# Kernel tuning notes

Hardware: AMD Instinct MI355X
Metric: run time of the kernel (lower is better)

## Reference

```python
import jax, jax.numpy as jnp
import numpy as np

DECAY = 0.99
EPSILON = 1e-05
COMMITMENT_COST = 0.25
N_TOKENS = 8192   # B * h * w = 8 * 32 * 32
EMBED_DIM = 4096
VOCAB = 8192


def setup_inputs() -> dict:
    key = jax.random.key(0)
    k1, k2, k3 = jax.random.split(key, 3)
    return {
        "inputs": jax.random.normal(k1, (N_TOKENS, EMBED_DIM), dtype=jnp.float32),
        "embedding": jax.random.normal(k2, (VOCAB, EMBED_DIM), dtype=jnp.float32),
        "ema_w": jax.random.normal(k3, (VOCAB, EMBED_DIM), dtype=jnp.float32),
        "ema_cluster_size": jnp.zeros((VOCAB,), dtype=jnp.float32),
    }


def reference(inputs, embedding, ema_w, ema_cluster_size):
    n_tokens = inputs.shape[0]
    vocab = embedding.shape[0]
    distances = (jnp.sum(inputs * inputs, axis=1, keepdims=True)
                 + jnp.sum(embedding * embedding, axis=1)
                 - 2.0 * jnp.matmul(inputs, embedding.T))
    encoding_indices = jnp.argmin(distances, axis=1)            # [N]
    # one-hot @ embedding == gather of codebook rows
    quantized = embedding[encoding_indices]                      # [N, D]
    # sum of one-hot encodings over tokens == per-code counts
    counts = jax.ops.segment_sum(jnp.ones((n_tokens,), inputs.dtype),
                                 encoding_indices, num_segments=vocab)  # [V]
    # EMA cluster-size update with Laplace smoothing
    new_cluster_size = ema_cluster_size * DECAY + (1.0 - DECAY) * counts
    n = jnp.sum(new_cluster_size)
    new_cluster_size = (new_cluster_size + EPSILON) / (n + vocab * EPSILON) * n
    # dw = encodings.T @ flat_input == scatter-add of inputs per code
    dw = jax.ops.segment_sum(inputs, encoding_indices, num_segments=vocab)  # [V, D]
    new_ema_w = ema_w * DECAY + (1.0 - DECAY) * dw
    new_embedding = new_ema_w / new_cluster_size[:, None]
    # commitment loss (codebook side detached)
    e_latent_loss = jnp.mean((jax.lax.stop_gradient(quantized) - inputs) ** 2)
    loss = COMMITMENT_COST * e_latent_loss
    # straight-through estimator
    quantized_st = inputs + jax.lax.stop_gradient(quantized - inputs)
    avg_probs = counts / n_tokens
    perplexity = jnp.exp(-jnp.sum(avg_probs * jnp.log(avg_probs + 1e-10)))
    return (loss, quantized_st, perplexity, encoding_indices[:, None],
            new_cluster_size, new_ema_w, new_embedding)
```

## Files before the change

### kernel.cpp

```cpp
#include <hip/hip_runtime.h>
#include <hip/hip_fp16.h>
#include <stdint.h>

typedef _Float16 f16;
typedef float f32x4 __attribute__((ext_vector_type(4)));
typedef int i32x4v __attribute__((ext_vector_type(4)));
typedef int i32x8v __attribute__((ext_vector_type(8)));
typedef unsigned long long u64;

#define N_TOK 8192
#define VOCAB 8192
#define DIM   4096
#define DELTA 64.0f

__device__ __forceinline__ void gload16(const void* g, void* l) {
    __builtin_amdgcn_global_load_lds(
        (const __attribute__((address_space(1))) unsigned int*)(uintptr_t)g,
        (__attribute__((address_space(3))) unsigned int*)(uintptr_t)l,
        16, 0, 0);
}

__device__ __forceinline__ float keyinv(unsigned k) {
    unsigned b = (k & 0x80000000u) ? (k ^ 0x80000000u) : ~k;
    return __uint_as_float(b);
}

__device__ __forceinline__ void ins2(u64& k1, u64& k2, u64 v) {
    if (v < k1) { k2 = k1; k1 = v; }
    else if (v < k2) { k2 = v; }
}

__global__ __launch_bounds__(256) void k_pack(const float* __restrict__ inputs,
                                              const float* __restrict__ embedding,
                                              char* __restrict__ apk, char* __restrict__ bpk,
                                              float* __restrict__ enorms,
                                              int* __restrict__ counts) {
    int b = blockIdx.x, t = threadIdx.x;
    bool isB = b >= N_TOK;
    int row = isB ? b - N_TOK : b;
    const float* src = (isB ? embedding : inputs) + (size_t)row * DIM;
    char* dst = (isB ? bpk : apk) + (size_t)row * DIM;
    double nrm = 0.0;
#pragma unroll
    for (int k = 0; k < 4; k++) {
        int d0 = t * 4 + 1024 * k;
        float4 v = *(const float4*)(src + d0);
        nrm += (double)v.x * v.x + (double)v.y * v.y
             + (double)v.z * v.z + (double)v.w * v.w;
        int packed = 0;
        packed = __builtin_amdgcn_cvt_pk_fp8_f32(v.x, v.y, packed, false);
        packed = __builtin_amdgcn_cvt_pk_fp8_f32(v.z, v.w, packed, true);
        int c = d0 & 127;
        int u = c >> 4;
        int p = ((u & 1) << 2) | (u >> 1);
        *(int*)(dst + (d0 & ~127) + (p << 4) + (c & 15)) = packed;
    }
    if (isB) {
        __shared__ double red[256];
        red[t] = nrm;
        __syncthreads();
        for (int off = 128; off > 0; off >>= 1) {
            if (t < off) red[t] += red[t + off];
            __syncthreads();
        }
        if (t == 0) {
            enorms[row] = (float)red[0];
            counts[row] = 0;
        }
    }
}

__global__ __launch_bounds__(256) void k_gemm(const char* __restrict__ apk,
                                              const char* __restrict__ bpk,
                                              const float* __restrict__ enorms,
                                              u64* __restrict__ cand) {
    __shared__ alignas(16) char lds[65536];
    int b = blockIdx.x;
    int x = b & 7, l = b >> 3;
    int bm = x * 8 + ((l >> 3) & 7);
    int bn = (l >> 6) * 8 + (l & 7);
    int tid = threadIdx.x;
    int lane = tid & 63, wid = tid >> 6;
    int wm = wid >> 1, wn = wid & 1;

    const char* srcs[8];
    unsigned lof[8];
#pragma unroll
    for (int e = 0; e < 8; e++) {
        int tile = e >> 2, q = e & 3;
        int s = q * 256 + tid;
        int r = s >> 3;
        int c16 = (s & 7) ^ (r & 7);
        int row = (tile ? bn : bm) * 128 + r;
        srcs[e] = (tile ? bpk : apk) + (size_t)row * DIM + c16 * 16;
        lof[e] = tile * 16384 + q * 4096 + wid * 1024;
    }

    f32x4 acc[4][4];
#pragma unroll
    for (int m = 0; m < 4; m++)
#pragma unroll
        for (int n = 0; n < 4; n++) acc[m][n] = (f32x4){0.f, 0.f, 0.f, 0.f};

    const int g = lane >> 4;
    const int ra = wm * 64 + (lane & 15);
    const int rb = wn * 64 + (lane & 15);

#define STAGE(buf) { _Pragma("unroll") for (int e = 0; e < 8; e++) { \
        gload16(srcs[e], &lds[(buf) * 32768u + lof[e]]); srcs[e] += 128; } }

    STAGE(0);

    for (int kt = 0; kt < 32; ++kt) {
        const unsigned cur = (kt & 1) ? 32768u : 0u;
        if (kt < 31) {
            STAGE((kt & 1) ^ 1);
            asm volatile("s_waitcnt vmcnt(8)" ::: "memory");
        } else {
            asm volatile("s_waitcnt vmcnt(0)" ::: "memory");
        }
        __builtin_amdgcn_sched_barrier(0);
        __builtin_amdgcn_s_barrier();
        __builtin_amdgcn_s_setprio(1);
        {
            i32x8v a8[4], b8[4];
#pragma unroll
            for (int m = 0; m < 4; m++) {
                int r = ra + m * 16;
                i32x4v lo = *(const i32x4v*)&lds[cur + r * 128 + ((g ^ (r & 7)) << 4)];
                i32x4v hi = *(const i32x4v*)&lds[cur + r * 128 + (((4 + g) ^ (r & 7)) << 4)];
                a8[m] = __builtin_shufflevector(lo, hi, 0, 1, 2, 3, 4, 5, 6, 7);
            }
#pragma unroll
            for (int n = 0; n < 4; n++) {
                int r = rb + n * 16;
                i32x4v lo = *(const i32x4v*)&lds[cur + 16384 + r * 128 + ((g ^ (r & 7)) << 4)];
                i32x4v hi = *(const i32x4v*)&lds[cur + 16384 + r * 128 + (((4 + g) ^ (r & 7)) << 4)];
                b8[n] = __builtin_shufflevector(lo, hi, 0, 1, 2, 3, 4, 5, 6, 7);
            }
#pragma unroll
            for (int m = 0; m < 4; m++)
#pragma unroll
                for (int n = 0; n < 4; n++)
                    acc[m][n] = __builtin_amdgcn_mfma_scale_f32_16x16x128_f8f6f4(
                        a8[m], b8[n], acc[m][n], 0, 0,
                        0, 0x7F7F7F7F, 0, 0x7F7F7F7F);
        }
        __builtin_amdgcn_s_setprio(0);
        __builtin_amdgcn_s_barrier();
    }
#undef STAGE

    float en[4];
    int colb = bn * 128 + wn * 64 + (lane & 15);
#pragma unroll
    for (int n = 0; n < 4; n++) en[n] = enorms[colb + n * 16];
#pragma unroll
    for (int m = 0; m < 4; m++) {
#pragma unroll
        for (int reg = 0; reg < 4; reg++) {
            u64 k1 = ~0ull, k2 = ~0ull;
#pragma unroll
            for (int n = 0; n < 4; n++) {
                float d = en[n] - 2.0f * acc[m][n][reg];
                unsigned bb = __float_as_uint(d);
                unsigned key = (bb & 0x80000000u) ? ~bb : (bb | 0x80000000u);
                ins2(k1, k2, ((u64)key << 32) | (unsigned)(colb + n * 16));
            }
#pragma unroll
            for (int msk = 1; msk < 16; msk <<= 1) {
                u64 o1 = __shfl_xor(k1, msk, 64);
                u64 o2 = __shfl_xor(k2, msk, 64);
                ins2(k1, k2, o1);
                ins2(k1, k2, o2);
            }
            if ((lane & 15) == 0) {
                int rowg = bm * 128 + wm * 64 + m * 16 + ((lane >> 4) << 2) + reg;
                size_t slot = ((size_t)rowg * 64 + bn) * 2 + wn;
                ulonglong2 v; v.x = k1; v.y = k2;
                *(ulonglong2*)&cand[slot * 2] = v;
            }
        }
    }
}

__global__ __launch_bounds__(256) void k_cand(const u64* __restrict__ cand,
                                              const float* __restrict__ enorms,
                                              const float* __restrict__ inputs,
                                              const float* __restrict__ embedding,
                                              float* __restrict__ o_idx,
                                              float* __restrict__ o_quant,
                                              float* __restrict__ partials,
                                              int* __restrict__ counts) {
    int tok = blockIdx.x, t = threadIdx.x;
    int lane = t & 63, w = t >> 6;
    __shared__ u64 redu[4];
    __shared__ float redf[4];
    __shared__ float pdot[64][4];
    __shared__ int clist[64];
    __shared__ int s_cnt;
    if (t == 0) s_cnt = 0;
    u64 e = cand[(size_t)tok * 256 + t];
    u64 v = e;
#pragma unroll
    for (int msk = 1; msk < 64; msk <<= 1) {
        u64 o = __shfl_xor(v, msk, 64);
        if (o < v) v = o;
    }
    if (lane == 0) redu[w] = v;
    __syncthreads();
    u64 m01 = redu[0] < redu[1] ? redu[0] : redu[1];
    u64 m23 = redu[2] < redu[3] ? redu[2] : redu[3];
    u64 mall = m01 < m23 ? m01 : m23;
    float dmin = keyinv((unsigned)(mall >> 32));
    float myd = keyinv((unsigned)(e >> 32));
    if (myd <= dmin + DELTA) {
        int p = atomicAdd(&s_cnt, 1);
        if (p < 64) clist[p] = (int)(unsigned)(e & 0xffffffffu);
    }
    __syncthreads();
    int nc = min(s_cnt, 64);

    const float* xrow = inputs + (size_t)tok * DIM;
    float4 xr4[4];
#pragma unroll
    for (int k = 0; k < 4; k++) xr4[k] = *(const float4*)(xrow + t * 4 + 1024 * k);

    for (int i = 0; i < nc; i++) {
        int c = clist[i];
        const float* erow = embedding + (size_t)c * DIM;
        float p = 0.f;
#pragma unroll
        for (int k = 0; k < 4; k++) {
            float4 e4 = *(const float4*)(erow + t * 4 + 1024 * k);
            p += xr4[k].x * e4.x + xr4[k].y * e4.y + xr4[k].z * e4.z + xr4[k].w * e4.w;
        }
#pragma unroll
        for (int msk = 1; msk < 64; msk <<= 1) p += __shfl_xor(p, msk, 64);
        if (lane == 0) pdot[i][w] = p;
    }
    __syncthreads();

    float best = 3.4e38f;
    int bcol = 0x7fffffff;
    for (int i = 0; i < nc; i++) {
        int c = clist[i];
        float dot = (pdot[i][0] + pdot[i][1]) + (pdot[i][2] + pdot[i][3]);
        float dist = enorms[c] - 2.0f * dot;
        if (dist < best || (dist == best && c < bcol)) { best = dist; bcol = c; }
    }
    const float* eb = embedding + (size_t)bcol * DIM;
    float* qrow = o_quant + (size_t)tok * DIM;
    float ls = 0.f;
#pragma unroll
    for (int k = 0; k < 4; k++) {
        int d = t * 4 + 1024 * k;
        float4 q4 = *(const float4*)(eb + d);
        qrow[d + 0] = q4.x; qrow[d + 1] = q4.y; qrow[d + 2] = q4.z; qrow[d + 3] = q4.w;
        float dx = q4.x - xr4[k].x, dy = q4.y - xr4[k].y;
        float dz = q4.z - xr4[k].z, dw = q4.w - xr4[k].w;
        ls += dx * dx + dy * dy + dz * dz + dw * dw;
    }
#pragma unroll
    for (int msk = 1; msk < 64; msk <<= 1) ls += __shfl_xor(ls, msk, 64);
    if (lane == 0) redf[w] = ls;
    __syncthreads();
    if (t == 0) {
        partials[tok] = (redf[0] + redf[1]) + (redf[2] + redf[3]);
        o_idx[tok] = (float)bcol;
        atomicAdd(&counts[bcol], 1);
    }
}

__global__ __launch_bounds__(1024) void k_cs(const int* __restrict__ counts,
                                             const float* __restrict__ ema_cs,
                                             float* __restrict__ o_ncs,
                                             float* __restrict__ o_perp) {
    __shared__ float red[1024];
    int t = threadIdx.x;
    float pre[8];
    float psum = 0.f, esum = 0.f;
#pragma unroll
    for (int k = 0; k < 8; k++) {
        int j = t * 8 + k;
        float c = (float)counts[j];
        float p = ema_cs[j] * 0.99f + 0.01f * c;
        pre[k] = p;
        psum += p;
        float ap = c * (1.0f / 8192.0f);
        esum += ap * logf(ap + 1e-10f);
    }
    red[t] = psum;
    __syncthreads();
    for (int off = 512; off > 0; off >>= 1) {
        if (t < off) red[t] += red[t + off];
        __syncthreads();
    }
    float n = red[0];
    __syncthreads();
    red[t] = esum;
    __syncthreads();
    for (int off = 512; off > 0; off >>= 1) {
        if (t < off) red[t] += red[t + off];
        __syncthreads();
    }
    if (t == 0) o_perp[0] = expf(-red[0]);
    float scale = n / (n + (float)VOCAB * 1e-5f);
#pragma unroll
    for (int k = 0; k < 8; k++) {
        int j = t * 8 + k;
        o_ncs[j] = (pre[k] + 1e-5f) * scale;
    }
}

__global__ __launch_bounds__(1024) void k_loss(const float* __restrict__ partials,
                                               float* __restrict__ o_loss) {
    __shared__ float red[1024];
    int t = threadIdx.x;
    float s = 0.f;
#pragma unroll
    for (int k = 0; k < 8; k++) s += partials[t * 8 + k];
    red[t] = s;
    __syncthreads();
    for (int off = 512; off > 0; off >>= 1) {
        if (t < off) red[t] += red[t + off];
        __syncthreads();
    }
    if (t == 0) o_loss[0] = 0.25f * red[0] / ((float)N_TOK * (float)DIM);
}

__global__ __launch_bounds__(256) void k_ema(const float* __restrict__ o_idx,
                                             const float* __restrict__ inputs,
                                             const float* __restrict__ ema_w,
                                             const float* __restrict__ o_ncs,
                                             float* __restrict__ o_neww,
                                             float* __restrict__ o_newemb) {
    int j = blockIdx.x, t = threadIdx.x;
    __shared__ int scan[256];
    __shared__ int list[256];
    __shared__ int s_total;
    int c = 0;
    for (int k = 0; k < 32; k++) {
        int tok = t * 32 + k;
        if ((int)o_idx[tok] == j) c++;
    }
    scan[t] = c;
    __syncthreads();
    for (int off = 1; off < 256; off <<= 1) {
        int add = (t >= off) ? scan[t - off] : 0;
        __syncthreads();
        scan[t] += add;
        __syncthreads();
    }
    int excl = scan[t] - c;
    if (t == 255) s_total = scan[255];
    __syncthreads();
    int pos = excl;
    for (int k = 0; k < 32; k++) {
        int tok = t * 32 + k;
        if ((int)o_idx[tok] == j && pos < 256) list[pos++] = tok;
    }
    __syncthreads();
    int total = s_total;
    float nc = o_ncs[j];
    size_t rowoff = (size_t)j * DIM;
#pragma unroll
    for (int k = 0; k < 4; k++) {
        int d = t * 4 + 1024 * k;
        float sx = 0.f, sy = 0.f, sz = 0.f, sw = 0.f;
        for (int q = 0; q < total; q++) {
            float4 v = *(const float4*)(inputs + (size_t)list[q] * DIM + d);
            sx += v.x; sy += v.y; sz += v.z; sw += v.w;
        }
        float4 w4 = *(const float4*)(ema_w + rowoff + d);
        float w0 = w4.x * 0.99f + 0.01f * sx;
        float w1 = w4.y * 0.99f + 0.01f * sy;
        float w2 = w4.z * 0.99f + 0.01f * sz;
        float w3 = w4.w * 0.99f + 0.01f * sw;
        o_neww[rowoff + d + 0] = w0; o_newemb[rowoff + d + 0] = w0 / nc;
        o_neww[rowoff + d + 1] = w1; o_newemb[rowoff + d + 1] = w1 / nc;
        o_neww[rowoff + d + 2] = w2; o_newemb[rowoff + d + 2] = w2 / nc;
        o_neww[rowoff + d + 3] = w3; o_newemb[rowoff + d + 3] = w3 / nc;
    }
}

extern "C" void kernel_launch(void* const* d_in, const int* in_sizes, int n_in,
                              void* d_out, int out_size, void* d_ws, size_t ws_size,
                              hipStream_t stream) {
    const float* inputs    = (const float*)d_in[0];
    const float* embedding = (const float*)d_in[1];
    const float* ema_w     = (const float*)d_in[2];
    const float* ema_cs    = (const float*)d_in[3];

    float* out = (float*)d_out;
    char* base = (char*)d_out;

    char* apk       = base;
    char* bpk       = base + 33554432;
    u64* cand       = (u64*)(base + 167772160);
    float* enorms   = (float*)(base + 184549376);
    int* counts     = (int*)(base + 184582144);
    float* partials = (float*)(base + 184614912);

    float* o_loss   = out;
    float* o_quant  = out + 1;
    float* o_perp   = out + 33554433;
    float* o_idx    = out + 33554434;
    float* o_ncs    = out + 33562626;
    float* o_neww   = out + 33570818;
    float* o_newemb = out + 67125250;

    k_pack<<<dim3(N_TOK + VOCAB), dim3(256), 0, stream>>>(inputs, embedding, apk, bpk,
                                                          enorms, counts);
    k_gemm<<<dim3(4096), dim3(256), 0, stream>>>(apk, bpk, enorms, cand);
    k_cand<<<dim3(N_TOK), dim3(256), 0, stream>>>(cand, enorms, inputs, embedding,
                                                  o_idx, o_quant, partials, counts);
    k_cs<<<dim3(1), dim3(1024), 0, stream>>>(counts, ema_cs, o_ncs, o_perp);
    k_loss<<<dim3(1), dim3(1024), 0, stream>>>(partials, o_loss);
    k_ema<<<dim3(VOCAB), dim3(256), 0, stream>>>(o_idx, inputs, ema_w, o_ncs, o_neww, o_newemb);
}
```

Before: 1.332 ms.

## Replace double-buffered FP8 GEMM K-loop with single-buffer 256-wide K tiles

The FP8 distance GEMM drops its two-stage LDS double buffer (128-byte K slices, explicit vmcnt waits, setprio) in favour of a single buffer holding 256-byte K slices. Each iteration loads the A and B tiles, synchronises, runs two MFMA half-steps, and synchronises again. This halves the loop count and barrier pairs and simplifies address arithmetic through a shared A/B pointer delta. In exchange, global loads no longer overlap with MFMA compute, so each iteration waits for its full load before computing.

```diff
diff --git a/kernel.cpp b/kernel.cpp
--- a/kernel.cpp
+++ b/kernel.cpp
@@ -87,14 +87,14 @@
     unsigned lof[8];
 #pragma unroll
     for (int e = 0; e < 8; e++) {
-        int tile = e >> 2, q = e & 3;
-        int s = q * 256 + tid;
-        int r = s >> 3;
-        int c16 = (s & 7) ^ (r & 7);
-        int row = (tile ? bn : bm) * 128 + r;
-        srcs[e] = (tile ? bpk : apk) + (size_t)row * DIM + c16 * 16;
-        lof[e] = tile * 16384 + q * 4096 + wid * 1024;
-    }
+        int s = e * 256 + tid;
+        int r = s >> 4;
+        int u = s & 15, h = u >> 3, j = u & 7;
+        int jp = j ^ (r & 7);
+        srcs[e] = apk + (size_t)(bm * 128 + r) * DIM + h * 128 + jp * 16;
+        lof[e] = e * 4096 + wid * 1024;
+    }
+    const ptrdiff_t bdelta = (bpk + (size_t)bn * 128 * DIM) - (apk + (size_t)bm * 128 * DIM);
 
     f32x4 acc[4][4];
 #pragma unroll
@@ -106,36 +106,29 @@
     const int ra = wm * 64 + (lane & 15);
     const int rb = wn * 64 + (lane & 15);
 
-#define STAGE(buf) { _Pragma("unroll") for (int e = 0; e < 8; e++) { \
-        gload16(srcs[e], &lds[(buf) * 32768u + lof[e]]); srcs[e] += 128; } }
-
-    STAGE(0);
-
-    for (int kt = 0; kt < 32; ++kt) {
-        const unsigned cur = (kt & 1) ? 32768u : 0u;
-        if (kt < 31) {
-            STAGE((kt & 1) ^ 1);
-            asm volatile("s_waitcnt vmcnt(8)" ::: "memory");
-        } else {
-            asm volatile("s_waitcnt vmcnt(0)" ::: "memory");
-        }
-        __builtin_amdgcn_sched_barrier(0);
-        __builtin_amdgcn_s_barrier();
-        __builtin_amdgcn_s_setprio(1);
-        {
+    for (int kt = 0; kt < 16; ++kt) {
+#pragma unroll
+        for (int e = 0; e < 8; e++) {
+            gload16(srcs[e], &lds[lof[e]]);
+            gload16(srcs[e] + bdelta, &lds[32768 + lof[e]]);
+            srcs[e] += 256;
+        }
+        __syncthreads();
+#pragma unroll
+        for (int h = 0; h < 2; h++) {
             i32x8v a8[4], b8[4];
 #pragma unroll
             for (int m = 0; m < 4; m++) {
                 int r = ra + m * 16;
-                i32x4v lo = *(const i32x4v*)&lds[cur + r * 128 + ((g ^ (r & 7)) << 4)];
-                i32x4v hi = *(const i32x4v*)&lds[cur + r * 128 + (((4 + g) ^ (r & 7)) << 4)];
+                i32x4v lo = *(const i32x4v*)&lds[r * 256 + h * 128 + ((g ^ (r & 7)) << 4)];
+                i32x4v hi = *(const i32x4v*)&lds[r * 256 + h * 128 + (((4 + g) ^ (r & 7)) << 4)];
                 a8[m] = __builtin_shufflevector(lo, hi, 0, 1, 2, 3, 4, 5, 6, 7);
             }
 #pragma unroll
             for (int n = 0; n < 4; n++) {
                 int r = rb + n * 16;
-                i32x4v lo = *(const i32x4v*)&lds[cur + 16384 + r * 128 + ((g ^ (r & 7)) << 4)];
-                i32x4v hi = *(const i32x4v*)&lds[cur + 16384 + r * 128 + (((4 + g) ^ (r & 7)) << 4)];
+                i32x4v lo = *(const i32x4v*)&lds[32768 + r * 256 + h * 128 + ((g ^ (r & 7)) << 4)];
+                i32x4v hi = *(const i32x4v*)&lds[32768 + r * 256 + h * 128 + (((4 + g) ^ (r & 7)) << 4)];
                 b8[n] = __builtin_shufflevector(lo, hi, 0, 1, 2, 3, 4, 5, 6, 7);
             }
 #pragma unroll
@@ -146,10 +139,8 @@
                         a8[m], b8[n], acc[m][n], 0, 0,
                         0, 0x7F7F7F7F, 0, 0x7F7F7F7F);
         }
-        __builtin_amdgcn_s_setprio(0);
-        __builtin_amdgcn_s_barrier();
-    }
-#undef STAGE
+        __syncthreads();
+    }
 
     float en[4];
     int colb = bn * 128 + wn * 64 + (lane & 15);
```

New measurement: 1.327 ms. No clear change (-0.4%).
